# Kernel optimization log

Measured on AMD Instinct MI355X. Metric: run time of the kernel, lower is better.

Reference implementation:

```python
import jax, jax.numpy as jnp
import numpy as np

TOP_K_PCT = 0.1
MAX_SHARP_TOKENS = 10
SMOOTHING = 0.1


def setup_inputs() -> dict:
    key = jax.random.key(0)
    logits = jax.random.normal(key, (2, 8, 2048, 2048), dtype=jnp.float32)
    return {"logits": logits, "dim": 3}


def reference(logits, dim):
    # Move the softmax axis to the end so lax.top_k / row-scatter apply.
    x = jnp.moveaxis(logits, dim, -1)
    N = x.shape[-1]
    k = min(MAX_SHARP_TOKENS, max(1, int(N * TOP_K_PCT)))

    vals, idx = jax.lax.top_k(x, k)            # [..., k], sorted descending
    topk_soft = jax.nn.softmax(vals, axis=-1)  # softmax over just the top-k values

    flat = x.reshape(-1, N)                    # [R, N]
    fidx = idx.reshape(-1, k)                  # [R, k]
    rows = jnp.arange(flat.shape[0])[:, None]

    # boolean mask of top-k positions
    mask = jnp.zeros(flat.shape, dtype=bool).at[rows, fidx].set(True)

    # softmax over the remaining (non-top-k) logits; top-k filled with dtype min
    neg_inf = jnp.finfo(flat.dtype).min
    remaining = jnp.where(mask, neg_inf, flat)
    rem_soft = jax.nn.softmax(remaining, axis=-1)
    rem_soft = jnp.where(mask, jnp.zeros((), flat.dtype), rem_soft)

    # scatter top-k softmax back, then blend
    final = jnp.zeros_like(flat).at[rows, fidx].set(topk_soft.reshape(-1, k))
    out = final * (1.0 - SMOOTHING) + rem_soft * SMOOTHING

    return jnp.moveaxis(out.reshape(x.shape), -1, dim)
```

## Files before the change

kernel.cpp:

```cpp
#include <hip/hip_runtime.h>
#include <math.h>

#define ROW_N 2048
#define KSEL 10
#define WCAP 64
#define RPW  4

typedef float f32x4 __attribute__((ext_vector_type(4)));
typedef unsigned long long u64;

__global__ __launch_bounds__(256) void topk_softmax_kernel(
    const float* __restrict__ in, float* __restrict__ out, int nw)
{
    const int lane = threadIdx.x & 63;
    const int wave = threadIdx.x >> 6;
    const int wid  = blockIdx.x * 4 + wave;

    __shared__ u64 s_cand[4][WCAP];

    f32x4 A[8], B[8];

    auto loadrow = [&](f32x4 (&V)[8], int row) {
        const f32x4* p = reinterpret_cast<const f32x4*>(in + (size_t)row * ROW_N);
        #pragma unroll
        for (int j = 0; j < 8; ++j) V[j] = p[j * 64 + lane];
    };

    auto process = [&](f32x4 (&V)[8], int row) {
        const size_t rbase = (size_t)row * ROW_N;

        float s = 0.f, q = 0.f, vm = -INFINITY;
        #pragma unroll
        for (int j = 0; j < 8; ++j)
            #pragma unroll
            for (int c = 0; c < 4; ++c) {
                float x = V[j][c];
                s += x; q = fmaf(x, x, q); vm = fmaxf(vm, x);
            }
        #pragma unroll
        for (int off = 32; off > 0; off >>= 1) {
            s += __shfl_xor(s, off);
            q += __shfl_xor(q, off);
            vm = fmaxf(vm, __shfl_xor(vm, off));
        }
        const float mu    = s * (1.f / ROW_N);
        const float sig   = sqrtf(fmaxf(q * (1.f / ROW_N) - mu * mu, 1e-20f));
        const float shift = fmaf(4.f, sig, mu);
        float Tf = fmaf(2.2f, sig, mu);

        int C = 0;
        #pragma unroll 1
        for (int t = 0; t < 8; ++t) {
            C = 0;
            #pragma unroll
            for (int j = 0; j < 8; ++j)
                #pragma unroll
                for (int c = 0; c < 4; ++c) {
                    bool cond = V[j][c] > Tf;
                    u64 m = __ballot(cond);
                    if (cond) {
                        int idx = j * 256 + lane * 4 + c;
                        uint32_t u  = __float_as_uint(V[j][c]);
                        uint32_t ov = u ^ ((uint32_t)((int32_t)u >> 31) | 0x80000000u);
                        int pos = C + (int)__builtin_amdgcn_mbcnt_hi(
                                          (unsigned)(m >> 32),
                                          __builtin_amdgcn_mbcnt_lo((unsigned)m, 0u));
                        if (pos < WCAP)
                            s_cand[wave][pos] = ((u64)ov << 16) |
                                                (unsigned)(2047 - idx);
                    }
                    C += __popcll(m);
                }
            if (C >= KSEL && C <= WCAP) break;
            Tf += (C < KSEL) ? (-0.5f * sig) : (0.5f * sig);
        }
        if (C > WCAP) C = WCAP;

        u64 k0 = (lane < C) ? s_cand[wave][lane] : 0ULL;

        float tot = 0.f;
        #pragma unroll
        for (int j = 0; j < 8; ++j) {
            f32x4 e;
            #pragma unroll
            for (int c = 0; c < 4; ++c) { e[c] = __expf(V[j][c] - shift); tot += e[c]; }
            V[j] = e;
        }
        #pragma unroll
        for (int off = 32; off > 0; off >>= 1) tot += __shfl_xor(tot, off);

        u64 kmin = 0ULL;
        #pragma unroll 1
        for (int b = 47; b >= 0; --b) {
            u64 trial = kmin | (1ULL << b);
            u64 mm = __ballot(k0 >= trial);
            if (__popcll(mm) >= KSEL) kmin = trial;
        }

        uint32_t ovk = (uint32_t)(k0 >> 16);
        float val = __uint_as_float(ovk ^ ((ovk & 0x80000000u) ? 0x80000000u
                                                              : 0xFFFFFFFFu));
        const bool win = (lane < C) && (k0 >= kmin);
        float ee = win ? __expf(val - vm) : 0.f;
        float ssum = ee;
        #pragma unroll
        for (int off = 32; off > 0; off >>= 1) ssum += __shfl_xor(ssum, off);

        const float tsum = ssum * __expf(vm - shift);
        const float aa   = 0.9f / ssum;
        const float bb   = 0.1f / (tot - tsum);

        f32x4* o4 = reinterpret_cast<f32x4*>(out + rbase);
        #pragma unroll
        for (int j = 0; j < 8; ++j) {
            f32x4 o;
            #pragma unroll
            for (int c = 0; c < 4; ++c) o[c] = V[j][c] * bb;
            __builtin_nontemporal_store(o, o4 + j * 64 + lane);
        }

        asm volatile("s_waitcnt vmcnt(0)" ::: "memory");
        if (win) out[rbase + (2047 - (int)(k0 & 0xFFFFull))] = ee * aa;
    };

    loadrow(A, wid);
    #pragma unroll 1
    for (int r = 0; r < RPW; r += 2) {
        loadrow(B, wid + (r + 1) * nw);
        process(A, wid + r * nw);
        if (r + 2 < RPW) loadrow(A, wid + (r + 2) * nw);
        process(B, wid + (r + 1) * nw);
    }
}

extern "C" void kernel_launch(void* const* d_in, const int* in_sizes, int n_in,
                              void* d_out, int out_size, void* d_ws, size_t ws_size,
                              hipStream_t stream) {
    const float* logits = (const float*)d_in[0];
    float* out = (float*)d_out;
    const int rows = out_size / ROW_N;
    const int nw = rows / RPW;
    topk_softmax_kernel<<<dim3(nw / 4), dim3(256), 0, stream>>>(logits, out, nw);
}
```

Before: 472.9 us.

## Process one row per wave, drop mean/variance stats, fast 32-bit radix threshold

```diff
diff --git a/kernel.cpp b/kernel.cpp
--- a/kernel.cpp
+++ b/kernel.cpp
@@ -4,133 +4,119 @@
 #define ROW_N 2048
 #define KSEL 10
 #define WCAP 64
-#define RPW  4
 
 typedef float f32x4 __attribute__((ext_vector_type(4)));
 typedef unsigned long long u64;
 
-__global__ __launch_bounds__(256) void topk_softmax_kernel(
-    const float* __restrict__ in, float* __restrict__ out, int nw)
+__global__ __launch_bounds__(256, 8) void topk_softmax_kernel(
+    const float* __restrict__ in, float* __restrict__ out)
 {
     const int lane = threadIdx.x & 63;
     const int wave = threadIdx.x >> 6;
-    const int wid  = blockIdx.x * 4 + wave;
+    const size_t base = ((size_t)blockIdx.x * 4 + wave) * ROW_N;
 
     __shared__ u64 s_cand[4][WCAP];
 
-    f32x4 A[8], B[8];
+    const f32x4* p4 = reinterpret_cast<const f32x4*>(in + base);
+    f32x4 V[8];
+    #pragma unroll
+    for (int j = 0; j < 8; ++j) V[j] = p4[j * 64 + lane];
 
-    auto loadrow = [&](f32x4 (&V)[8], int row) {
-        const f32x4* p = reinterpret_cast<const f32x4*>(in + (size_t)row * ROW_N);
+    float vm = -INFINITY;
+    #pragma unroll
+    for (int j = 0; j < 8; ++j)
         #pragma unroll
-        for (int j = 0; j < 8; ++j) V[j] = p[j * 64 + lane];
-    };
+        for (int c = 0; c < 4; ++c) vm = fmaxf(vm, V[j][c]);
+    #pragma unroll
+    for (int off = 32; off > 0; off >>= 1) vm = fmaxf(vm, __shfl_xor(vm, off));
 
-    auto process = [&](f32x4 (&V)[8], int row) {
-        const size_t rbase = (size_t)row * ROW_N;
-
-        float s = 0.f, q = 0.f, vm = -INFINITY;
+    const int low0 = 2047 - lane * 4;
+    float Tf = 2.2f;
+    float dlt = 0.35f;
+    int C = 0;
+    #pragma unroll 1
+    for (int t = 0; t < 8; ++t) {
+        C = 0;
         #pragma unroll
         for (int j = 0; j < 8; ++j)
             #pragma unroll
             for (int c = 0; c < 4; ++c) {
-                float x = V[j][c];
-                s += x; q = fmaf(x, x, q); vm = fmaxf(vm, x);
+                bool cond = V[j][c] > Tf;
+                u64 m = __ballot(cond);
+                if (cond) {
+                    uint32_t u  = __float_as_uint(V[j][c]);
+                    uint32_t ov = u ^ ((uint32_t)((int32_t)u >> 31) | 0x80000000u);
+                    int pos = C + (int)__builtin_amdgcn_mbcnt_hi(
+                                      (unsigned)(m >> 32),
+                                      __builtin_amdgcn_mbcnt_lo((unsigned)m, 0u));
+                    if (pos < WCAP)
+                        s_cand[wave][pos] =
+                            ((u64)ov << 16) | (unsigned)(low0 - (j * 256 + c));
+                }
+                C += __popcll(m);
             }
+        if (C >= KSEL && C <= WCAP) break;
+        Tf += (C < KSEL) ? -dlt : dlt;
+        dlt *= 2.f;
+    }
+    if (C > WCAP) C = WCAP;
+
+    u64 k0 = (lane < C) ? s_cand[wave][lane] : 0ULL;
+    const uint32_t ov0 = (uint32_t)(k0 >> 16);
+
+    const float K  = 1.4426950408889634f;
+    const float c0 = -vm * K;
+    float tot = 0.f;
+    #pragma unroll
+    for (int j = 0; j < 8; ++j) {
+        f32x4 e;
         #pragma unroll
-        for (int off = 32; off > 0; off >>= 1) {
-            s += __shfl_xor(s, off);
-            q += __shfl_xor(q, off);
-            vm = fmaxf(vm, __shfl_xor(vm, off));
-        }
-        const float mu    = s * (1.f / ROW_N);
-        const float sig   = sqrtf(fmaxf(q * (1.f / ROW_N) - mu * mu, 1e-20f));
-        const float shift = fmaf(4.f, sig, mu);
-        float Tf = fmaf(2.2f, sig, mu);
+        for (int c = 0; c < 4; ++c) { e[c] = exp2f(fmaf(V[j][c], K, c0)); tot += e[c]; }
+        V[j] = e;
+    }
 
-        int C = 0;
-        #pragma unroll 1
-        for (int t = 0; t < 8; ++t) {
-            C = 0;
-            #pragma unroll
-            for (int j = 0; j < 8; ++j)
-                #pragma unroll
-                for (int c = 0; c < 4; ++c) {
-                    bool cond = V[j][c] > Tf;
-                    u64 m = __ballot(cond);
-                    if (cond) {
-                        int idx = j * 256 + lane * 4 + c;
-                        uint32_t u  = __float_as_uint(V[j][c]);
-                        uint32_t ov = u ^ ((uint32_t)((int32_t)u >> 31) | 0x80000000u);
-                        int pos = C + (int)__builtin_amdgcn_mbcnt_hi(
-                                          (unsigned)(m >> 32),
-                                          __builtin_amdgcn_mbcnt_lo((unsigned)m, 0u));
-                        if (pos < WCAP)
-                            s_cand[wave][pos] = ((u64)ov << 16) |
-                                                (unsigned)(2047 - idx);
-                    }
-                    C += __popcll(m);
-                }
-            if (C >= KSEL && C <= WCAP) break;
-            Tf += (C < KSEL) ? (-0.5f * sig) : (0.5f * sig);
-        }
-        if (C > WCAP) C = WCAP;
-
-        u64 k0 = (lane < C) ? s_cand[wave][lane] : 0ULL;
-
-        float tot = 0.f;
-        #pragma unroll
-        for (int j = 0; j < 8; ++j) {
-            f32x4 e;
-            #pragma unroll
-            for (int c = 0; c < 4; ++c) { e[c] = __expf(V[j][c] - shift); tot += e[c]; }
-            V[j] = e;
-        }
-        #pragma unroll
-        for (int off = 32; off > 0; off >>= 1) tot += __shfl_xor(tot, off);
-
-        u64 kmin = 0ULL;
+    uint32_t kov = 0;
+    #pragma unroll
+    for (int b = 31; b >= 0; --b) {
+        uint32_t trial = kov | (1u << b);
+        if (__popcll(__ballot(ov0 >= trial)) >= KSEL) kov = trial;
+    }
+    u64 kmin = ((u64)kov) << 16;
+    int W = __popcll(__ballot(ov0 >= kov));
+    if (W != KSEL) {
+        kmin = 0ULL;
         #pragma unroll 1
         for (int b = 47; b >= 0; --b) {
             u64 trial = kmin | (1ULL << b);
-            u64 mm = __ballot(k0 >= trial);
-            if (__popcll(mm) >= KSEL) kmin = trial;
+            if (__popcll(__ballot(k0 >= trial)) >= KSEL) kmin = trial;
         }
+    }
+    const bool win = (k0 >= kmin) && (k0 != 0ULL);
 
-        uint32_t ovk = (uint32_t)(k0 >> 16);
-        float val = __uint_as_float(ovk ^ ((ovk & 0x80000000u) ? 0x80000000u
-                                                              : 0xFFFFFFFFu));
-        const bool win = (lane < C) && (k0 >= kmin);
-        float ee = win ? __expf(val - vm) : 0.f;
-        float ssum = ee;
+    uint32_t bits = ov0 ^ ((ov0 & 0x80000000u) ? 0x80000000u : 0xFFFFFFFFu);
+    float val = __uint_as_float(bits);
+    float ee  = win ? exp2f(fmaf(val, K, c0)) : 0.f;
+
+    float ssum = ee;
+    #pragma unroll
+    for (int off = 32; off > 0; off >>= 1) {
+        tot  += __shfl_xor(tot, off);
+        ssum += __shfl_xor(ssum, off);
+    }
+
+    const float aa = 0.9f / ssum;
+    const float bb = 0.1f / (tot - ssum);
+
+    f32x4* o4 = reinterpret_cast<f32x4*>(out + base);
+    #pragma unroll
+    for (int j = 0; j < 8; ++j) {
+        f32x4 o;
         #pragma unroll
-        for (int off = 32; off > 0; off >>= 1) ssum += __shfl_xor(ssum, off);
-
-        const float tsum = ssum * __expf(vm - shift);
-        const float aa   = 0.9f / ssum;
-        const float bb   = 0.1f / (tot - tsum);
-
-        f32x4* o4 = reinterpret_cast<f32x4*>(out + rbase);
-        #pragma unroll
-        for (int j = 0; j < 8; ++j) {
-            f32x4 o;
-            #pragma unroll
-            for (int c = 0; c < 4; ++c) o[c] = V[j][c] * bb;
-            __builtin_nontemporal_store(o, o4 + j * 64 + lane);
-        }
-
-        asm volatile("s_waitcnt vmcnt(0)" ::: "memory");
-        if (win) out[rbase + (2047 - (int)(k0 & 0xFFFFull))] = ee * aa;
-    };
-
-    loadrow(A, wid);
-    #pragma unroll 1
-    for (int r = 0; r < RPW; r += 2) {
-        loadrow(B, wid + (r + 1) * nw);
-        process(A, wid + r * nw);
-        if (r + 2 < RPW) loadrow(A, wid + (r + 2) * nw);
-        process(B, wid + (r + 1) * nw);
+        for (int c = 0; c < 4; ++c) o[c] = V[j][c] * bb;
+        __builtin_nontemporal_store(o, o4 + j * 64 + lane);
     }
+    asm volatile("s_waitcnt vmcnt(0)" ::: "memory");
+    if (win) out[base + 2047 - (int)(k0 & 0xFFFFull)] = ee * aa;
 }
 
 extern "C" void kernel_launch(void* const* d_in, const int* in_sizes, int n_in,
@@ -139,6 +125,5 @@
     const float* logits = (const float*)d_in[0];
     float* out = (float*)d_out;
     const int rows = out_size / ROW_N;
-    const int nw = rows / RPW;
-    topk_softmax_kernel<<<dim3(nw / 4), dim3(256), 0, stream>>>(logits, out, nw);
+    topk_softmax_kernel<<<dim3(rows / 4), dim3(256), 0, stream>>>(logits, out);
 }
```

Measured after the change: 598.0 us. 26.5% more time.
